# Kernel optimization log

Hardware: AMD Instinct MI355X
Metric: run time of the kernel (lower is better)

Reference implementation:

```python
import jax, jax.numpy as jnp
import numpy as np

# dims: F=N_fault, V=N_train (noise samples), E=batch, M=n_in+2, N=n_out
F, V, E, N_IN, N_OUT = 2, 4, 2048, 512, 512
M = N_IN + 2
GMIN, GMAX, EPS_TRAIN, PGMIN = 0.01, 10.0, 0.1, 1e-4
ETA2_ACT1 = 0.20  # ACT1.eta_fault[0,2], used in theta init
# pTanh activation params per ACT: a = e0 + e1*tanh((z-e2)*e3)
ETAS = np.array([[0.05, 0.90, 0.20, 8.0],
                 [0.10, 0.80, 0.30, 5.0],
                 [0.00, 1.00, 0.25, 10.0],
                 [0.15, 0.70, 0.15, 6.0]], dtype=np.float32)


def setup_inputs() -> dict:
    key = jax.random.key(0)
    k1, k2, k3, k4, k5 = jax.random.split(key, 5)
    a_previous = jax.random.uniform(k1, (F, V, E, N_IN), jnp.float32)
    # theta init per __init__: rand/100 + gmin; last row += gmax; row -2 from eta_2 formula
    theta = jax.random.uniform(k2, (M, N_OUT), jnp.float32) / 100.0 + GMIN
    theta = theta.at[-1, :].add(GMAX)
    theta = theta.at[-2, :].set(ETA2_ACT1 / (1.0 - ETA2_ACT1) * (jnp.sum(theta[:-2, :], 0) + theta[-1, :]))
    cofficients_act = jax.random.uniform(k3, (4, N_OUT), jnp.float32)
    noise_u = jax.random.uniform(k4, (F, V, M, N_OUT), jnp.float32)   # theta_noisy uniform draw
    gumbel_u = jax.random.uniform(k5, (4, N_OUT), jnp.float32)        # gumbel uniform draw
    return {"a_previous": a_previous, "theta_": theta,
            "cofficients_act": cofficients_act, "noise_u": noise_u, "gumbel_u": gumbel_u}


def _forward(a_previous, theta_, cofficients_act, noise_u, gumbel_u):
    sg = jax.lax.stop_gradient
    # --- theta property: clamp to [-gmax,gmax], zero |.|<gmin, straight-through ---
    th_c = jnp.clip(theta_, -GMAX, GMAX)
    th_t = jnp.where(jnp.abs(th_c) < GMIN, 0.0, th_c)
    theta = sg(th_t) + theta_ - sg(theta_)
    # --- theta_noisy: multiplicative uniform noise in [1-eps, 1+eps]; FaultMask == 1 ---
    theta_noisy = theta[None, None] * ((noise_u * 2.0 - 1.0) * EPS_TRAIN + 1.0)  # [F,V,M,N]
    absn = jnp.abs(theta_noisy)
    W = absn / (jnp.sum(absn, axis=2, keepdims=True) + 1e-10)
    pos = (theta_noisy >= 0).astype(theta_noisy.dtype)
    neg = 1.0 - pos
    # --- MAC: extend input with [ones, zeros], inverter path, split-sign matmul ---
    ones = jnp.ones(a_previous.shape[:3] + (1,), a_previous.dtype)
    zeros = jnp.zeros_like(ones)
    x_ext = jnp.concatenate([a_previous, ones, zeros], axis=3)  # [F,V,E,M]
    x_neg = (-x_ext).at[..., -1].set(0.0)                       # ideal INV(a) = -a, last col zeroed
    z = (jnp.einsum('fvem,fvmn->fven', x_ext, W * pos)
         + jnp.einsum('fvem,fvmn->fven', x_neg, W * neg))       # [F,V,E,N]
    # --- MAC_power: vectorized form of the quad loop ---
    # Power = sum_{f,v,m,n} g[m,n] * sum_e (x_ext*pos + x_neg*neg - y)^2 / (E*V*F)
    # pos*neg = 0, pos^2 = pos  =>  expand the square into einsum reductions.
    g_init = jnp.abs(th_c)
    g_tilde = g_init * (PGMIN / jnp.min(g_init, axis=0, keepdims=True))
    pos_d, neg_d = sg(pos), sg(neg)  # detached in torch source
    sx2 = jnp.einsum('fvem,fvem->fvm', x_ext, x_ext)
    sn2 = jnp.einsum('fvem,fvem->fvm', x_neg, x_neg)
    sy2 = jnp.einsum('fven,fven->fvn', z, z)
    C = jnp.einsum('fvem,fven->fvmn', x_ext, z)
    D = jnp.einsum('fvem,fven->fvmn', x_neg, z)
    p1 = (jnp.einsum('fvm,fvmn,mn->', sx2, pos_d, g_tilde)
          + jnp.einsum('fvm,fvmn,mn->', sn2, neg_d, g_tilde))
    p2 = -2.0 * (jnp.einsum('fvmn,fvmn,mn->', C, pos_d, g_tilde)
                 + jnp.einsum('fvmn,fvmn,mn->', D, neg_d, g_tilde))
    p3 = jnp.einsum('fvn,n->', sy2, jnp.sum(g_tilde, axis=0))
    mac_power = (p1 + p2 + p3) / (E * V * F)
    # --- CoFF_ACT: clamped logits + gumbel, softmax, hard argmax straight-through ---
    c = cofficients_act + sg(jnp.clip(cofficients_act, -1.0, 1.0) - cofficients_act)
    gn = -jnp.log(-jnp.log(gumbel_u + 1e-20) + 1e-20)
    alpha = jax.nn.softmax((c + gn) / 1.0, axis=0)              # temperature = 1.0
    hard = jax.nn.one_hot(jnp.argmax(alpha, axis=0), 4, axis=0, dtype=alpha.dtype)
    alpha_st = sg(hard) + alpha - sg(alpha)                      # [4, N]
    # --- mix the four pTanh activations ---
    a_new = jnp.zeros_like(z)
    for i in range(4):
        e0, e1, e2, e3 = ETAS[i]
        a_new = a_new + alpha_st[i] * (e0 + e1 * jnp.tanh((z - e2) * e3))
    return a_new, mac_power


def reference(a_previous, theta_, cofficients_act, noise_u, gumbel_u):
    return _forward(a_previous, theta_, cofficients_act, noise_u, gumbel_u)
```

## Files before the change

kernel.cpp:

```cpp
#include <hip/hip_runtime.h>

typedef unsigned short u16;
typedef __attribute__((ext_vector_type(8))) short short8;
typedef __attribute__((ext_vector_type(4))) float f32x4;

#define NF 2
#define NV 4
#define FV 8
#define NE 2048
#define NIN 512
#define NOUT 512
#define NM 514

#define WS_P1      0u
#define WS_P2      2048u
#define WS_P3      3072u
#define WS_SCALE   4096u
#define WS_G       6144u
#define WS_GN      8320u
#define WS_ETA     10368u
#define WS_BIASZ   18560u
#define WS_BIAST   34944u
#define WS_DENP    51328u
#define WS_PMIN    182400u
#define WS_PSUM    313472u
#define WS_ABF     444544u
#define WS_BZT     17221760u
#define WS_BTT     21416064u

__constant__ float c_etas[4][4] = {
    {0.05f, 0.90f, 0.20f, 8.0f},
    {0.10f, 0.80f, 0.30f, 5.0f},
    {0.00f, 1.00f, 0.25f, 10.0f},
    {0.15f, 0.70f, 0.15f, 6.0f}};

__device__ __forceinline__ u16 f2bf(float x) {
    unsigned u = __float_as_uint(x);
    unsigned r = (u + 0x7fffu + ((u >> 16) & 1u)) >> 16;
    return (u16)r;
}

__device__ __forceinline__ void gll16(const void* g, void* l) {
    __builtin_amdgcn_global_load_lds((__attribute__((address_space(1))) void*)g,
                                     (__attribute__((address_space(3))) void*)l,
                                     16, 0, 0);
}

__global__ void kA_part(const float* __restrict__ theta_, float* __restrict__ pmin,
                        float* __restrict__ psum) {
    int t = threadIdx.x;
    int n2 = t * 2;
    int r0 = blockIdx.x * 9;
    float mn0 = 3.4e38f, mn1 = 3.4e38f, s0 = 0.f, s1 = 0.f;
    int rend = r0 + 9;
    if (rend > NM) rend = NM;
    for (int r = r0; r < rend; r++) {
        float2 v = *(const float2*)(theta_ + r * NOUT + n2);
        float a0 = fabsf(fminf(fmaxf(v.x, -10.f), 10.f));
        float a1 = fabsf(fminf(fmaxf(v.y, -10.f), 10.f));
        mn0 = fminf(mn0, a0); mn1 = fminf(mn1, a1);
        s0 += a0; s1 += a1;
    }
    *(float2*)(pmin + blockIdx.x * NOUT + n2) = make_float2(mn0, mn1);
    *(float2*)(psum + blockIdx.x * NOUT + n2) = make_float2(s0, s1);
}

__global__ void kB_fold(const float* __restrict__ pmin, const float* __restrict__ psum,
                        const float* __restrict__ coeff, const float* __restrict__ gumb,
                        float* __restrict__ scale, float* __restrict__ Gn,
                        float4* __restrict__ eta4) {
    int n = threadIdx.x;
    float mn = 3.4e38f, s = 0.f;
    for (int i = 0; i < 64; i++) {
        mn = fminf(mn, pmin[i * NOUT + n]);
        s += psum[i * NOUT + n];
    }
    float sc = 1e-4f / mn;
    scale[n] = sc;
    Gn[n] = sc * s;
    float best = -1e30f;
    int bi = 0;
    for (int i = 0; i < 4; i++) {
        float c = fminf(fmaxf(coeff[i * NOUT + n], -1.f), 1.f);
        float u = gumb[i * NOUT + n];
        float g = -logf(-logf(u + 1e-20f) + 1e-20f);
        float v = c + g;
        if (v > best) { best = v; bi = i; }
    }
    eta4[n] = make_float4(c_etas[bi][0], c_etas[bi][1], c_etas[bi][2], c_etas[bi][3]);
}

__global__ void kC_grow(const float* __restrict__ theta_, const float* __restrict__ scale,
                        float* __restrict__ G) {
    int m = blockIdx.x;
    int t = threadIdx.x;
    const float4* rowp = (const float4*)(theta_ + m * NOUT);
    const float4* scp = (const float4*)scale;
    float acc = 0.f;
#pragma unroll
    for (int i = 0; i < 2; i++) {
        float4 v = rowp[t * 2 + i];
        float4 s = scp[t * 2 + i];
        acc += fabsf(fminf(fmaxf(v.x, -10.f), 10.f)) * s.x
             + fabsf(fminf(fmaxf(v.y, -10.f), 10.f)) * s.y
             + fabsf(fminf(fmaxf(v.z, -10.f), 10.f)) * s.z
             + fabsf(fminf(fmaxf(v.w, -10.f), 10.f)) * s.w;
    }
    for (int off = 32; off > 0; off >>= 1) acc += __shfl_down(acc, off);
    if (t == 0) G[m] = acc;
}

__global__ void k_denomp(const float* __restrict__ theta_, const float* __restrict__ noise,
                         float* __restrict__ denomp) {
    const int fv = blockIdx.z, mc = blockIdx.y, nc = blockIdx.x;
    const int t = threadIdx.x;
    const int nq = t & 15, mr = t >> 4;
    const int nb = nc * 64 + nq * 4;
    float4 acc = {0.f, 0.f, 0.f, 0.f};
#pragma unroll
    for (int i = 0; i < 4; i++) {
        int m = mc * 64 + mr + i * 16;
        float4 th4 = *(const float4*)(theta_ + m * NOUT + nb);
        float4 no4 = *(const float4*)(noise + (fv * NM + m) * NOUT + nb);
#define DACC(c) { float fac = no4.c * 0.2f + 0.9f; \
                  float thc = fminf(fmaxf(th4.c, -10.f), 10.f); \
                  float tht = (fabsf(thc) < 0.01f) ? 0.f : thc; \
                  acc.c += fabsf(tht * fac); }
        DACC(x) DACC(y) DACC(z) DACC(w)
#undef DACC
    }
    __shared__ float4 red[16][17];
    red[mr][nq] = acc;
    __syncthreads();
    if (t < 16) {
        float4 s = red[0][t];
#pragma unroll
        for (int r = 1; r < 16; r++) {
            float4 v = red[r][t];
            s.x += v.x; s.y += v.y; s.z += v.z; s.w += v.w;
        }
        *(float4*)(denomp + (mc * 8 + fv) * NOUT + nc * 64 + t * 4) = s;
    }
}

__global__ void k_wmat3(const float* __restrict__ theta_, const float* __restrict__ scale,
                        const float* __restrict__ noise,
                        u16* __restrict__ BzT, u16* __restrict__ BtT,
                        float* __restrict__ bias_z, float* __restrict__ bias_t) {
    const int nt = blockIdx.x, mt = blockIdx.y, fv = blockIdx.z;
    const int t = threadIdx.x;
    const int nq = t & 15, mr = t >> 4;
    const int nb = nt * 64 + nq * 4;
    __shared__ u16 Wl[64][72];
    __shared__ u16 Sl[64][72];
    float4 sc4 = *(const float4*)(scale + nb);
#pragma unroll
    for (int i = 0; i < 4; i++) {
        int ml = mr + i * 16;
        int m = mt * 64 + ml;
        float4 th4 = *(const float4*)(theta_ + m * NOUT + nb);
        float4 no4 = *(const float4*)(noise + (fv * NM + m) * NOUT + nb);
        ushort4 wv, sv;
#define WCOMP(c, fld) { float fac = no4.c * 0.2f + 0.9f; \
                        float thc = fminf(fmaxf(th4.c, -10.f), 10.f); \
                        float gi = fabsf(thc); \
                        float tht = (gi < 0.01f) ? 0.f : thc; \
                        float th = tht * fac; \
                        wv.fld = f2bf(th); \
                        sv.fld = f2bf(((th >= 0.f) ? 1.f : -1.f) * gi * sc4.c); }
        WCOMP(x, x) WCOMP(y, y) WCOMP(z, z) WCOMP(w, w)
#undef WCOMP
        *(ushort4*)(&Wl[ml][nq * 4]) = wv;
        *(ushort4*)(&Sl[ml][nq * 4]) = sv;
    }
    __syncthreads();
    const int mb = (t & 15) * 4;
#pragma unroll
    for (int r = 0; r < 4; r++) {
        int nl = (t >> 4) + r * 16;
        ushort4 wv, sv;
        wv.x = Wl[mb][nl]; wv.y = Wl[mb + 1][nl]; wv.z = Wl[mb + 2][nl]; wv.w = Wl[mb + 3][nl];
        sv.x = Sl[mb][nl]; sv.y = Sl[mb + 1][nl]; sv.z = Sl[mb + 2][nl]; sv.w = Sl[mb + 3][nl];
        int gidx = (fv * NOUT + nt * 64 + nl) * NIN + mt * 64 + mb;
        *(ushort4*)(BzT + gidx) = wv;
        *(ushort4*)(BtT + gidx) = sv;
    }
    if (mt == 0 && t < 64) {
        int n = nt * 64 + t;
        float fac = noise[(fv * NM + 512) * NOUT + n] * 0.2f + 0.9f;
        float thc = fminf(fmaxf(theta_[512 * NOUT + n], -10.f), 10.f);
        float gi = fabsf(thc);
        float tht = (gi < 0.01f) ? 0.f : thc;
        float th = tht * fac;
        bias_z[fv * NOUT + n] = th;
        bias_t[fv * NOUT + n] = ((th >= 0.f) ? 1.f : -1.f) * gi * scale[n];
    }
}

__global__ void k_prepA(const float* __restrict__ a_prev, const float* __restrict__ G,
                        u16* __restrict__ Abf, float* __restrict__ p1slot) {
    int t = threadIdx.x;
    float acc = 0.f;
#pragma unroll
    for (int i = 0; i < 4; i++) {
        int idx = (i * 2048 + blockIdx.x) * 256 + t;
        float4 v = ((const float4*)a_prev)[idx];
        int k = (idx & 127) << 2;
        float4 g4 = *((const float4*)(G + k));
        acc += v.x * v.x * g4.x + v.y * v.y * g4.y + v.z * v.z * g4.z + v.w * v.w * g4.w;
        ushort4 o;
        o.x = f2bf(v.x); o.y = f2bf(v.y); o.z = f2bf(v.z); o.w = f2bf(v.w);
        ((ushort4*)Abf)[idx] = o;
    }
    for (int off = 32; off > 0; off >>= 1) acc += __shfl_down(acc, off);
    __shared__ float red[4];
    int lane = t & 63, wv = t >> 6;
    if (lane == 0) red[wv] = acc;
    __syncthreads();
    if (t == 0)
        atomicAdd(&p1slot[(blockIdx.x & 63) * 8], red[0] + red[1] + red[2] + red[3]);
}

__global__ __launch_bounds__(256, 2) void k_gemm(
    const u16* __restrict__ Abf, const u16* __restrict__ BzT, const u16* __restrict__ BtT,
    const float* __restrict__ bias_z, const float* __restrict__ bias_t,
    const float* __restrict__ Gn, const float4* __restrict__ eta4,
    const float* __restrict__ theta_, const float* __restrict__ noise,
    const float* __restrict__ denomp,
    float* __restrict__ out, float* __restrict__ p2slot, float* __restrict__ p3slot) {
    __shared__ alignas(16) u16 As[128 * 64];
    __shared__ alignas(16) u16 Bzs[128 * 64];
    __shared__ alignas(16) u16 Bts[128 * 64];
    const int tid = threadIdx.x;
    const int lane = tid & 63;
    const int wv = tid >> 6;
    const int wr = wv >> 1, wc = wv & 1;
    const int fv = blockIdx.z;
    const int e0 = blockIdx.y * 128;
    const int n0 = blockIdx.x * 128;

    const u16* Ag = Abf + (fv * NE + e0) * NIN;
    const u16* Bzg = BzT + (fv * NOUT + n0) * NIN;
    const u16* Btg = BtT + (fv * NOUT + n0) * NIN;

    f32x4 accz[4][4], acct[4][4];
#pragma unroll
    for (int i = 0; i < 4; i++)
#pragma unroll
        for (int j = 0; j < 4; j++) {
            f32x4 zz = {0.f, 0.f, 0.f, 0.f};
            accz[i][j] = zz;
            acct[i][j] = zz;
        }

    const int srow = tid >> 3;
    const int swz = (((tid & 7) ^ (srow & 7))) * 8;

    for (int k0 = 0; k0 < 512; k0 += 64) {
#pragma unroll
        for (int i = 0; i < 4; i++) {
            int so = (i * 32 + srow) * 512 + k0 + swz;
            int dof = i * 2048 + tid * 8;
            gll16(Ag + so, (u16*)As + dof);
            gll16(Bzg + so, (u16*)Bzs + dof);
            gll16(Btg + so, (u16*)Bts + dof);
        }
        __builtin_amdgcn_s_waitcnt(0);
        __syncthreads();
        const int rA = wr * 64 + (lane & 15);
        const int rB = wc * 64 + (lane & 15);
#pragma unroll
        for (int s = 0; s < 2; s++) {
            const int ca = ((s * 4 + (lane >> 4)) ^ (lane & 7)) * 8;
            short8 af[4], bzf[4], btf[4];
#pragma unroll
            for (int i = 0; i < 4; i++) af[i] = *(const short8*)(As + (rA + i * 16) * 64 + ca);
#pragma unroll
            for (int j = 0; j < 4; j++) {
                bzf[j] = *(const short8*)(Bzs + (rB + j * 16) * 64 + ca);
                btf[j] = *(const short8*)(Bts + (rB + j * 16) * 64 + ca);
            }
#pragma unroll
            for (int i = 0; i < 4; i++)
#pragma unroll
                for (int j = 0; j < 4; j++) {
                    accz[i][j] = __builtin_amdgcn_mfma_f32_16x16x32_bf16(af[i], bzf[j], accz[i][j], 0, 0, 0);
                    acct[i][j] = __builtin_amdgcn_mfma_f32_16x16x32_bf16(af[i], btf[j], acct[i][j], 0, 0, 0);
                }
        }
        __syncthreads();
    }

    float p2 = 0.f, p3 = 0.f;
    const int col = lane & 15;
    const int rowq = (lane >> 4) * 4;
#pragma unroll
    for (int j = 0; j < 4; j++) {
        int n = n0 + wc * 64 + j * 16 + col;
        float dsum = 1e-10f;
#pragma unroll
        for (int mc = 0; mc < 8; mc++) dsum += denomp[(mc * 8 + fv) * NOUT + n];
#pragma unroll
        for (int mx = 512; mx < 514; mx++) {
            float fac = noise[(fv * NM + mx) * NOUT + n] * 0.2f + 0.9f;
            float thc = fminf(fmaxf(theta_[mx * NOUT + n], -10.f), 10.f);
            float tht = (fabsf(thc) < 0.01f) ? 0.f : thc;
            dsum += fabsf(tht * fac);
        }
        float rdv = 1.f / dsum;
        float bz = bias_z[fv * NOUT + n];
        float bt = bias_t[fv * NOUT + n];
        float gnv = Gn[n];
        float4 e4 = eta4[n];
#pragma unroll
        for (int i = 0; i < 4; i++) {
            int ebase = e0 + wr * 64 + i * 16 + rowq;
#pragma unroll
            for (int r = 0; r < 4; r++) {
                float z = (accz[i][j][r] + bz) * rdv;
                float t = acct[i][j][r] + bt;
                p2 += z * t;
                p3 += z * z * gnv;
                float x = (z - e4.z) * e4.w;
                float ex = __expf(2.f * x);
                float th = 1.f - 2.f / (ex + 1.f);
                out[(fv * NE + ebase + r) * NOUT + n] = e4.x + e4.y * th;
            }
        }
    }
    for (int off = 32; off > 0; off >>= 1) {
        p2 += __shfl_down(p2, off);
        p3 += __shfl_down(p3, off);
    }
    __shared__ float r2[4], r3[4];
    if (lane == 0) { r2[wv] = p2; r3[wv] = p3; }
    __syncthreads();
    if (tid == 0) {
        int slot = ((blockIdx.x + blockIdx.y * 4 + blockIdx.z * 64) & 31) * 8;
        atomicAdd(&p2slot[slot], r2[0] + r2[1] + r2[2] + r2[3]);
        atomicAdd(&p3slot[slot], r3[0] + r3[1] + r3[2] + r3[3]);
    }
}

__global__ void k_final(const float* __restrict__ p1s, const float* __restrict__ p2s,
                        const float* __restrict__ p3s, const float* __restrict__ G,
                        float* __restrict__ out) {
    int t = threadIdx.x;
    float s1 = p1s[t * 8];
    float s2 = (t < 32) ? p2s[t * 8] : 0.f;
    float s3 = (t < 32) ? p3s[t * 8] : 0.f;
    for (int off = 32; off > 0; off >>= 1) {
        s1 += __shfl_down(s1, off);
        s2 += __shfl_down(s2, off);
        s3 += __shfl_down(s3, off);
    }
    if (t == 0) {
        float mp = (s1 + 16384.f * G[512] - 2.f * s2 + s3) * (1.f / 16384.f);
        out[8388608] = mp;
    }
}

extern "C" void kernel_launch(void* const* d_in, const int* in_sizes, int n_in,
                              void* d_out, int out_size, void* d_ws, size_t ws_size,
                              hipStream_t stream) {
    const float* a_prev = (const float*)d_in[0];
    const float* theta_ = (const float*)d_in[1];
    const float* coeff = (const float*)d_in[2];
    const float* noise = (const float*)d_in[3];
    const float* gumb = (const float*)d_in[4];
    float* out = (float*)d_out;
    char* w = (char*)d_ws;
    float* p1s = (float*)(w + WS_P1);
    float* p2s = (float*)(w + WS_P2);
    float* p3s = (float*)(w + WS_P3);
    float* scale = (float*)(w + WS_SCALE);
    float* G = (float*)(w + WS_G);
    float* Gn = (float*)(w + WS_GN);
    float4* eta4 = (float4*)(w + WS_ETA);
    float* bias_z = (float*)(w + WS_BIASZ);
    float* bias_t = (float*)(w + WS_BIAST);
    float* denomp = (float*)(w + WS_DENP);
    float* pmin = (float*)(w + WS_PMIN);
    float* psum = (float*)(w + WS_PSUM);
    u16* Abf = (u16*)(w + WS_ABF);
    u16* BzT = (u16*)(w + WS_BZT);
    u16* BtT = (u16*)(w + WS_BTT);

    hipMemsetAsync(w + WS_P1, 0, 4096, stream);

    kA_part<<<64, 256, 0, stream>>>(theta_, pmin, psum);
    kB_fold<<<1, 512, 0, stream>>>(pmin, psum, coeff, gumb, scale, Gn, eta4);
    kC_grow<<<514, 64, 0, stream>>>(theta_, scale, G);
    k_denomp<<<dim3(8, 8, FV), 256, 0, stream>>>(theta_, noise, denomp);
    k_wmat3<<<dim3(8, 8, FV), 256, 0, stream>>>(theta_, scale, noise,
                                                BzT, BtT, bias_z, bias_t);
    k_prepA<<<2048, 256, 0, stream>>>(a_prev, G, Abf, p1s);
    k_gemm<<<dim3(4, 16, FV), 256, 0, stream>>>(Abf, BzT, BtT, bias_z, bias_t, Gn, eta4,
                                                theta_, noise, denomp, out, p2s, p3s);
    k_final<<<1, 64, 0, stream>>>(p1s, p2s, p3s, G, out);
}
```

Before: 146.3 us.

## Fuse denominator pass into weight prep, drop memset and final kernel

The column-denominator partial sums are now computed inside k_wmat3, so the separate k_denomp launch and its second read of theta and noise go away. The per-column scale factor moves out of the bf16 B matrix and is applied in the GEMM epilogue. The final reduction is folded into the GEMM through a last-block atomic counter, and zeroing of the accumulation slots moves into kA_part, which removes the memset and k_final launches. Per-column epilogue constants are staged in shared memory. The trade-offs are a threadfence-based last-block pattern and a change in bf16 rounding of the scaled weights.

Result: slower. 154.4 us (+5.5%).

```diff
diff --git a/kernel.cpp b/kernel.cpp
--- a/kernel.cpp
+++ b/kernel.cpp
@@ -15,18 +15,19 @@
 #define WS_P1      0u
 #define WS_P2      2048u
 #define WS_P3      3072u
-#define WS_SCALE   4096u
-#define WS_G       6144u
-#define WS_GN      8320u
-#define WS_ETA     10368u
-#define WS_BIASZ   18560u
-#define WS_BIAST   34944u
-#define WS_DENP    51328u
-#define WS_PMIN    182400u
-#define WS_PSUM    313472u
-#define WS_ABF     444544u
-#define WS_BZT     17221760u
-#define WS_BTT     21416064u
+#define WS_CTR     4096u
+#define WS_SCALE   4224u
+#define WS_G       6272u
+#define WS_GN      8448u
+#define WS_ETA     10496u
+#define WS_BIASZ   18688u
+#define WS_BIAST   35072u
+#define WS_DENP    51456u
+#define WS_PMIN    182528u
+#define WS_PSUM    313600u
+#define WS_ABF     444672u
+#define WS_BZT     17221888u
+#define WS_BTT     21416192u
 
 __constant__ float c_etas[4][4] = {
     {0.05f, 0.90f, 0.20f, 8.0f},
@@ -47,8 +48,11 @@
 }
 
 __global__ void kA_part(const float* __restrict__ theta_, float* __restrict__ pmin,
-                        float* __restrict__ psum) {
+                        float* __restrict__ psum, float* __restrict__ wszero) {
     int t = threadIdx.x;
+    if (blockIdx.x == 0) {
+        for (int i = t; i < 1056; i += 256) wszero[i] = 0.f;
+    }
     int n2 = t * 2;
     int r0 = blockIdx.x * 9;
     float mn0 = 3.4e38f, mn1 = 3.4e38f, s0 = 0.f, s1 = 0.f;
@@ -110,50 +114,18 @@
     if (t == 0) G[m] = acc;
 }
 
-__global__ void k_denomp(const float* __restrict__ theta_, const float* __restrict__ noise,
-                         float* __restrict__ denomp) {
-    const int fv = blockIdx.z, mc = blockIdx.y, nc = blockIdx.x;
-    const int t = threadIdx.x;
-    const int nq = t & 15, mr = t >> 4;
-    const int nb = nc * 64 + nq * 4;
-    float4 acc = {0.f, 0.f, 0.f, 0.f};
-#pragma unroll
-    for (int i = 0; i < 4; i++) {
-        int m = mc * 64 + mr + i * 16;
-        float4 th4 = *(const float4*)(theta_ + m * NOUT + nb);
-        float4 no4 = *(const float4*)(noise + (fv * NM + m) * NOUT + nb);
-#define DACC(c) { float fac = no4.c * 0.2f + 0.9f; \
-                  float thc = fminf(fmaxf(th4.c, -10.f), 10.f); \
-                  float tht = (fabsf(thc) < 0.01f) ? 0.f : thc; \
-                  acc.c += fabsf(tht * fac); }
-        DACC(x) DACC(y) DACC(z) DACC(w)
-#undef DACC
-    }
-    __shared__ float4 red[16][17];
-    red[mr][nq] = acc;
-    __syncthreads();
-    if (t < 16) {
-        float4 s = red[0][t];
-#pragma unroll
-        for (int r = 1; r < 16; r++) {
-            float4 v = red[r][t];
-            s.x += v.x; s.y += v.y; s.z += v.z; s.w += v.w;
-        }
-        *(float4*)(denomp + (mc * 8 + fv) * NOUT + nc * 64 + t * 4) = s;
-    }
-}
-
-__global__ void k_wmat3(const float* __restrict__ theta_, const float* __restrict__ scale,
-                        const float* __restrict__ noise,
+__global__ void k_wmat3(const float* __restrict__ theta_, const float* __restrict__ noise,
                         u16* __restrict__ BzT, u16* __restrict__ BtT,
-                        float* __restrict__ bias_z, float* __restrict__ bias_t) {
+                        float* __restrict__ bias_z, float* __restrict__ bias_t,
+                        float* __restrict__ denomp) {
     const int nt = blockIdx.x, mt = blockIdx.y, fv = blockIdx.z;
     const int t = threadIdx.x;
     const int nq = t & 15, mr = t >> 4;
     const int nb = nt * 64 + nq * 4;
     __shared__ u16 Wl[64][72];
     __shared__ u16 Sl[64][72];
-    float4 sc4 = *(const float4*)(scale + nb);
+    __shared__ float4 red[16][17];
+    float4 dacc = {0.f, 0.f, 0.f, 0.f};
 #pragma unroll
     for (int i = 0; i < 4; i++) {
         int ml = mr + i * 16;
@@ -167,13 +139,24 @@
                         float tht = (gi < 0.01f) ? 0.f : thc; \
                         float th = tht * fac; \
                         wv.fld = f2bf(th); \
-                        sv.fld = f2bf(((th >= 0.f) ? 1.f : -1.f) * gi * sc4.c); }
+                        sv.fld = f2bf((th >= 0.f) ? gi : -gi); \
+                        dacc.c += fabsf(th); }
         WCOMP(x, x) WCOMP(y, y) WCOMP(z, z) WCOMP(w, w)
 #undef WCOMP
         *(ushort4*)(&Wl[ml][nq * 4]) = wv;
         *(ushort4*)(&Sl[ml][nq * 4]) = sv;
     }
+    red[mr][nq] = dacc;
     __syncthreads();
+    if (t < 16) {
+        float4 s = red[0][t];
+#pragma unroll
+        for (int r = 1; r < 16; r++) {
+            float4 v = red[r][t];
+            s.x += v.x; s.y += v.y; s.z += v.z; s.w += v.w;
+        }
+        *(float4*)(denomp + (mt * 8 + fv) * NOUT + nt * 64 + t * 4) = s;
+    }
     const int mb = (t & 15) * 4;
 #pragma unroll
     for (int r = 0; r < 4; r++) {
@@ -193,7 +176,7 @@
         float tht = (gi < 0.01f) ? 0.f : thc;
         float th = tht * fac;
         bias_z[fv * NOUT + n] = th;
-        bias_t[fv * NOUT + n] = ((th >= 0.f) ? 1.f : -1.f) * gi * scale[n];
+        bias_t[fv * NOUT + n] = (th >= 0.f) ? gi : -gi;
     }
 }
 
@@ -226,8 +209,11 @@
     const float* __restrict__ bias_z, const float* __restrict__ bias_t,
     const float* __restrict__ Gn, const float4* __restrict__ eta4,
     const float* __restrict__ theta_, const float* __restrict__ noise,
-    const float* __restrict__ denomp,
-    float* __restrict__ out, float* __restrict__ p2slot, float* __restrict__ p3slot) {
+    const float* __restrict__ denomp, const float* __restrict__ scale,
+    const float* __restrict__ G,
+    float* __restrict__ out, float* __restrict__ p1slot,
+    float* __restrict__ p2slot, float* __restrict__ p3slot,
+    unsigned* __restrict__ ctr) {
     __shared__ alignas(16) u16 As[128 * 64];
     __shared__ alignas(16) u16 Bzs[128 * 64];
     __shared__ alignas(16) u16 Bts[128 * 64];
@@ -291,12 +277,14 @@
         __syncthreads();
     }
 
-    float p2 = 0.f, p3 = 0.f;
-    const int col = lane & 15;
-    const int rowq = (lane >> 4) * 4;
-#pragma unroll
-    for (int j = 0; j < 4; j++) {
-        int n = n0 + wc * 64 + j * 16 + col;
+    float* rdvl = (float*)As;
+    float* bzl = rdvl + 128;
+    float* btl = bzl + 128;
+    float* gnl = btl + 128;
+    float* scl = gnl + 128;
+    float4* e4l = (float4*)(scl + 128);
+    if (tid < 128) {
+        int n = n0 + tid;
         float dsum = 1e-10f;
 #pragma unroll
         for (int mc = 0; mc < 8; mc++) dsum += denomp[(mc * 8 + fv) * NOUT + n];
@@ -307,18 +295,35 @@
             float tht = (fabsf(thc) < 0.01f) ? 0.f : thc;
             dsum += fabsf(tht * fac);
         }
-        float rdv = 1.f / dsum;
-        float bz = bias_z[fv * NOUT + n];
-        float bt = bias_t[fv * NOUT + n];
-        float gnv = Gn[n];
-        float4 e4 = eta4[n];
+        rdvl[tid] = 1.f / dsum;
+        bzl[tid] = bias_z[fv * NOUT + n];
+        btl[tid] = bias_t[fv * NOUT + n];
+        gnl[tid] = Gn[n];
+        scl[tid] = scale[n];
+        e4l[tid] = eta4[n];
+    }
+    __syncthreads();
+
+    float p2 = 0.f, p3 = 0.f;
+    const int col = lane & 15;
+    const int rowq = (lane >> 4) * 4;
+#pragma unroll
+    for (int j = 0; j < 4; j++) {
+        int nli = wc * 64 + j * 16 + col;
+        int n = n0 + nli;
+        float rdv = rdvl[nli];
+        float bz = bzl[nli];
+        float bt = btl[nli];
+        float gnv = gnl[nli];
+        float sc = scl[nli];
+        float4 e4 = e4l[nli];
 #pragma unroll
         for (int i = 0; i < 4; i++) {
             int ebase = e0 + wr * 64 + i * 16 + rowq;
 #pragma unroll
             for (int r = 0; r < 4; r++) {
                 float z = (accz[i][j][r] + bz) * rdv;
-                float t = acct[i][j][r] + bt;
+                float t = (acct[i][j][r] + bt) * sc;
                 p2 += z * t;
                 p3 += z * z * gnv;
                 float x = (z - e4.z) * e4.w;
@@ -333,30 +338,32 @@
         p3 += __shfl_down(p3, off);
     }
     __shared__ float r2[4], r3[4];
+    __shared__ unsigned lastf;
     if (lane == 0) { r2[wv] = p2; r3[wv] = p3; }
     __syncthreads();
     if (tid == 0) {
         int slot = ((blockIdx.x + blockIdx.y * 4 + blockIdx.z * 64) & 31) * 8;
         atomicAdd(&p2slot[slot], r2[0] + r2[1] + r2[2] + r2[3]);
         atomicAdd(&p3slot[slot], r3[0] + r3[1] + r3[2] + r3[3]);
-    }
-}
-
-__global__ void k_final(const float* __restrict__ p1s, const float* __restrict__ p2s,
-                        const float* __restrict__ p3s, const float* __restrict__ G,
-                        float* __restrict__ out) {
-    int t = threadIdx.x;
-    float s1 = p1s[t * 8];
-    float s2 = (t < 32) ? p2s[t * 8] : 0.f;
-    float s3 = (t < 32) ? p3s[t * 8] : 0.f;
-    for (int off = 32; off > 0; off >>= 1) {
-        s1 += __shfl_down(s1, off);
-        s2 += __shfl_down(s2, off);
-        s3 += __shfl_down(s3, off);
-    }
-    if (t == 0) {
-        float mp = (s1 + 16384.f * G[512] - 2.f * s2 + s3) * (1.f / 16384.f);
-        out[8388608] = mp;
+        __threadfence();
+        unsigned c = atomicAdd(ctr, 1u);
+        lastf = (c == 511u) ? 1u : 0u;
+    }
+    __syncthreads();
+    if (lastf && tid < 64) {
+        __threadfence();
+        float s1 = p1slot[tid * 8];
+        float s2 = (tid < 32) ? p2slot[tid * 8] : 0.f;
+        float s3 = (tid < 32) ? p3slot[tid * 8] : 0.f;
+        for (int off = 32; off > 0; off >>= 1) {
+            s1 += __shfl_down(s1, off);
+            s2 += __shfl_down(s2, off);
+            s3 += __shfl_down(s3, off);
+        }
+        if (tid == 0) {
+            float mp = (s1 + 16384.f * G[512] - 2.f * s2 + s3) * (1.f / 16384.f);
+            out[8388608] = mp;
+        }
     }
 }
 
@@ -373,6 +380,7 @@
     float* p1s = (float*)(w + WS_P1);
     float* p2s = (float*)(w + WS_P2);
     float* p3s = (float*)(w + WS_P3);
+    unsigned* ctr = (unsigned*)(w + WS_CTR);
     float* scale = (float*)(w + WS_SCALE);
     float* G = (float*)(w + WS_G);
     float* Gn = (float*)(w + WS_GN);
@@ -386,16 +394,13 @@
     u16* BzT = (u16*)(w + WS_BZT);
     u16* BtT = (u16*)(w + WS_BTT);
 
-    hipMemsetAsync(w + WS_P1, 0, 4096, stream);
-
-    kA_part<<<64, 256, 0, stream>>>(theta_, pmin, psum);
+    kA_part<<<64, 256, 0, stream>>>(theta_, pmin, psum, (float*)w);
     kB_fold<<<1, 512, 0, stream>>>(pmin, psum, coeff, gumb, scale, Gn, eta4);
     kC_grow<<<514, 64, 0, stream>>>(theta_, scale, G);
-    k_denomp<<<dim3(8, 8, FV), 256, 0, stream>>>(theta_, noise, denomp);
-    k_wmat3<<<dim3(8, 8, FV), 256, 0, stream>>>(theta_, scale, noise,
-                                                BzT, BtT, bias_z, bias_t);
+    k_wmat3<<<dim3(8, 8, FV), 256, 0, stream>>>(theta_, noise, BzT, BtT,
+                                                bias_z, bias_t, denomp);
     k_prepA<<<2048, 256, 0, stream>>>(a_prev, G, Abf, p1s);
     k_gemm<<<dim3(4, 16, FV), 256, 0, stream>>>(Abf, BzT, BtT, bias_z, bias_t, Gn, eta4,
-                                                theta_, noise, denomp, out, p2s, p3s);
-    k_final<<<1, 64, 0, stream>>>(p1s, p2s, p3s, G, out);
-}
+                                                theta_, noise, denomp, scale, G,
+                                                out, p1s, p2s, p3s, ctr);
+}
```
